# Kernel optimization log

Measured on AMD Instinct MI355X. Metric: run time of the kernel, lower is better.

## Reference

```python
import jax, jax.numpy as jnp
import numpy as np

HEADS = 12
HEAD_DIM = 64  # dim=768 // heads=12
NEG = -1e9


def setup_inputs() -> dict:
    key = jax.random.key(0)
    k1, k2, k3 = jax.random.split(key, 3)
    dim = HEADS * HEAD_DIM
    x = jax.random.normal(k1, (8, 1024, dim), dtype=jnp.float32)
    W_qkv = jax.random.normal(k2, (dim, 3 * dim), dtype=jnp.float32) * (dim ** -0.5)
    b_qkv = jnp.zeros((3 * dim,), dtype=jnp.float32)
    W_out = jax.random.normal(k3, (dim, dim), dtype=jnp.float32) * (dim ** -0.5)
    b_out = jnp.zeros((dim,), dtype=jnp.float32)
    return {"x": x, "W_qkv": W_qkv, "b_qkv": b_qkv, "W_out": W_out, "b_out": b_out}


def reference(x, W_qkv, b_qkv, W_out, b_out):
    B, T, C = x.shape
    qkv = x @ W_qkv + b_qkv                      # [B,T,3C]
    q, k, v = jnp.split(qkv, 3, axis=-1)
    # [B,T,C] -> [B,H,T,Dh]
    def split_heads(t):
        return t.reshape(B, T, HEADS, HEAD_DIM).transpose(0, 2, 1, 3)
    q, k, v = split_heads(q), split_heads(k), split_heads(v)
    att = jnp.einsum('bhqd,bhkd->bhqk', q, k) / jnp.sqrt(jnp.float32(HEAD_DIM))
    causal = jnp.tril(jnp.ones((T, T), dtype=bool))  # [T,T]
    att = jnp.where(causal[None, None], att, NEG)
    att = jax.nn.softmax(att, axis=-1)
    out = jnp.einsum('bhqk,bhkd->bhqd', att, v)  # [B,H,T,Dh]
    out = out.transpose(0, 2, 1, 3).reshape(B, T, C)
    return out @ W_out + b_out
```

## Files before the change

kernel.cpp:

```cpp
#include <hip/hip_runtime.h>
#include <hip/hip_bf16.h>

typedef unsigned short u16;
typedef unsigned int u32;
typedef __attribute__((ext_vector_type(8))) short short8;
typedef __attribute__((ext_vector_type(4))) float f32x4;
typedef __attribute__((ext_vector_type(16))) float f32x16;
typedef __attribute__((ext_vector_type(4))) unsigned int uint4v;

__device__ __forceinline__ u16 f2bf(float f) {
    union { float f; unsigned int u; } v; v.f = f;
    unsigned int u = v.u;
    return (u16)((u + 0x7FFFu + ((u >> 16) & 1u)) >> 16);
}
__device__ __forceinline__ u32 pk2(float a, float b) {
    return ((u32)f2bf(b) << 16) | (u32)f2bf(a);
}

__global__ void k_convert(const float* __restrict__ x, u16* __restrict__ o, int n4) {
    int i = blockIdx.x * blockDim.x + threadIdx.x;
    if (i < n4) {
        float4 v = ((const float4*)x)[i];
        ushort4 r;
        r.x = f2bf(v.x); r.y = f2bf(v.y); r.z = f2bf(v.z); r.w = f2bf(v.w);
        ((ushort4*)o)[i] = r;
    }
}

__global__ void k_transpose_bf(const float* __restrict__ W, u16* __restrict__ Wt, int K, int N) {
    __shared__ u16 t[32][33];
    int n0 = blockIdx.x * 32, k0 = blockIdx.y * 32;
    int tx = threadIdx.x, ty = threadIdx.y;
    #pragma unroll
    for (int i = 0; i < 4; i++) {
        t[ty + i * 8][tx] = f2bf(W[(long)(k0 + ty + i * 8) * N + n0 + tx]);
    }
    __syncthreads();
    #pragma unroll
    for (int i = 0; i < 4; i++) {
        Wt[(long)(n0 + ty + i * 8) * K + k0 + tx] = t[tx][ty + i * 8];
    }
}

__global__ void k_vt(const u16* __restrict__ qkv, u16* __restrict__ vt) {
    __shared__ u16 s[32][33];
    int t0 = blockIdx.x * 32, d0 = blockIdx.y * 32, bh = blockIdx.z;
    int b = bh / 12, h = bh - b * 12;
    int tx = threadIdx.x, ty = threadIdx.y;
    const u16* src = qkv + (size_t)(b * 1024 + t0) * 2304 + 1536 + h * 64 + d0;
    #pragma unroll
    for (int i = 0; i < 4; i++) {
        s[ty + i * 8][tx] = src[(size_t)(ty + i * 8) * 2304 + tx];
    }
    __syncthreads();
    u16* dst = vt + (size_t)bh * 65536 + (size_t)d0 * 1024 + t0;
    #pragma unroll
    for (int i = 0; i < 4; i++) {
        dst[(size_t)(ty + i * 8) * 1024 + tx] = s[tx][ty + i * 8];
    }
}

template<int EPI>
__global__ __launch_bounds__(256) void k_gemm_bt(
    const u16* __restrict__ A, const u16* __restrict__ Bt, const float* __restrict__ bias,
    float* __restrict__ Cf, u16* __restrict__ Cb,
    int M, int N, int K)
{
    __shared__ u16 lA[128][40];
    __shared__ u16 lB[128][40];
    int tid = threadIdx.x;
    int wid = tid >> 6, lane = tid & 63;
    int wm = wid >> 1, wn = wid & 1;
    int ln = lane & 15, gp = lane >> 4;
    int gm0 = blockIdx.x * 128, gn0 = blockIdx.y * 128;

    f32x4 zf = {0.f, 0.f, 0.f, 0.f};
    f32x4 acc[4][4];
    #pragma unroll
    for (int i = 0; i < 4; i++)
        #pragma unroll
        for (int j = 0; j < 4; j++) acc[i][j] = zf;

    int sr = tid >> 2;
    int sc = (tid & 3) * 8;

    for (int k0 = 0; k0 < K; k0 += 32) {
        #pragma unroll
        for (int j = 0; j < 2; j++) {
            int r = sr + j * 64;
            *(uint4v*)&lA[r][sc] = *(const uint4v*)&A[(long)(gm0 + r) * K + k0 + sc];
            *(uint4v*)&lB[r][sc] = *(const uint4v*)&Bt[(long)(gn0 + r) * K + k0 + sc];
        }
        __syncthreads();
        short8 af[4], bfr[4];
        #pragma unroll
        for (int i = 0; i < 4; i++) {
            af[i]  = *(const short8*)&lA[wm * 64 + i * 16 + ln][gp * 8];
            bfr[i] = *(const short8*)&lB[wn * 64 + i * 16 + ln][gp * 8];
        }
        #pragma unroll
        for (int i = 0; i < 4; i++)
            #pragma unroll
            for (int j = 0; j < 4; j++)
                acc[i][j] = __builtin_amdgcn_mfma_f32_16x16x32_bf16(af[i], bfr[j], acc[i][j], 0, 0, 0);
        __syncthreads();
    }

    #pragma unroll
    for (int i = 0; i < 4; i++) {
        #pragma unroll
        for (int j = 0; j < 4; j++) {
            #pragma unroll
            for (int r = 0; r < 4; r++) {
                int m = gm0 + wm * 64 + i * 16 + gp * 4 + r;
                int n = gn0 + wn * 64 + j * 16 + ln;
                float v = acc[i][j][r] + bias[n];
                if (EPI == 0) Cf[(long)m * N + n] = v;
                else          Cb[(long)m * N + n] = f2bf(v);
            }
        }
    }
}

__global__ __launch_bounds__(64) void k_attn(
    const u16* __restrict__ qkv, const u16* __restrict__ Vt,
    u16* __restrict__ O)
{
    int lane = threadIdx.x;
    int l31 = lane & 31, hi = lane >> 5;
    int bx = blockIdx.x;
    int qtq = bx / 96, bh = bx - qtq * 96;
    int qt = 31 - qtq, q0 = qt * 32;
    int b = bh / 12, h = bh - b * 12;
    const u16* Qb  = qkv + (size_t)(b * 1024) * 2304 + h * 64;
    const u16* Kbb = Qb + 768;
    const u16* Vb  = Vt + (size_t)bh * 65536;

    short8 qf[4];
    #pragma unroll
    for (int ch = 0; ch < 4; ch++)
        qf[ch] = *(const short8*)&Qb[(size_t)(q0 + l31) * 2304 + ch * 16 + hi * 8];

    f32x16 o0 = {}, o1 = {};
    float mrun = -INFINITY, lsum = 0.f;
    const float SC = 0.18033688011f;

    int nit = qt + 1;
    for (int it = 0; it < nit; it++) {
        int kt = it * 32;
        f32x16 sa = {}, sb = {};
        {
            short8 kf0 = *(const short8*)&Kbb[(size_t)(kt + l31) * 2304 + 0 * 16 + hi * 8];
            short8 kf1 = *(const short8*)&Kbb[(size_t)(kt + l31) * 2304 + 1 * 16 + hi * 8];
            short8 kf2 = *(const short8*)&Kbb[(size_t)(kt + l31) * 2304 + 2 * 16 + hi * 8];
            short8 kf3 = *(const short8*)&Kbb[(size_t)(kt + l31) * 2304 + 3 * 16 + hi * 8];
            sa = __builtin_amdgcn_mfma_f32_32x32x16_bf16(kf0, qf[0], sa, 0, 0, 0);
            sb = __builtin_amdgcn_mfma_f32_32x32x16_bf16(kf2, qf[2], sb, 0, 0, 0);
            sa = __builtin_amdgcn_mfma_f32_32x32x16_bf16(kf1, qf[1], sa, 0, 0, 0);
            sb = __builtin_amdgcn_mfma_f32_32x32x16_bf16(kf3, qf[3], sb, 0, 0, 0);
        }
        float ps[16];
        int qg = q0 + l31;
        #pragma unroll
        for (int r = 0; r < 16; r++) {
            int krow = kt + (r & 3) + 8 * (r >> 2) + 4 * hi;
            ps[r] = (krow <= qg) ? (sa[r] + sb[r]) * SC : -1e30f;
        }
        float t8[8];
        #pragma unroll
        for (int i = 0; i < 8; i++) t8[i] = fmaxf(ps[i], ps[i + 8]);
        float t4a = fmaxf(t8[0], t8[1]), t4b = fmaxf(t8[2], t8[3]);
        float t4c = fmaxf(t8[4], t8[5]), t4d = fmaxf(t8[6], t8[7]);
        float tm = fmaxf(fmaxf(t4a, t4b), fmaxf(t4c, t4d));
        tm = fmaxf(tm, __shfl_xor(tm, 32));
        float mn = fmaxf(mrun, tm);
        float scale = exp2f(mrun - mn);
        mrun = mn;
        float rs = 0.f;
        #pragma unroll
        for (int r = 0; r < 16; r++) { ps[r] = exp2f(ps[r] - mn); rs += ps[r]; }
        rs += __shfl_xor(rs, 32);
        lsum = lsum * scale + rs;
        #pragma unroll
        for (int r = 0; r < 16; r++) { o0[r] *= scale; o1[r] *= scale; }
        u32 c[8], sw[8];
        #pragma unroll
        for (int i = 0; i < 8; i++) c[i] = pk2(ps[2 * i], ps[2 * i + 1]);
        #pragma unroll
        for (int i = 0; i < 8; i++) sw[i] = (u32)__shfl_xor((int)c[i], 32);
        union { u32 u[4]; short8 s8; } pb0, pb1;
        pb0.u[0] = hi ? sw[2] : c[0];
        pb0.u[1] = hi ? sw[3] : c[1];
        pb0.u[2] = hi ? c[2]  : sw[0];
        pb0.u[3] = hi ? c[3]  : sw[1];
        pb1.u[0] = hi ? sw[6] : c[4];
        pb1.u[1] = hi ? sw[7] : c[5];
        pb1.u[2] = hi ? c[6]  : sw[4];
        pb1.u[3] = hi ? c[7]  : sw[5];
        #pragma unroll
        for (int kh = 0; kh < 2; kh++) {
            const short8* pbp = kh ? &pb1.s8 : &pb0.s8;
            short8 vf0 = *(const short8*)&Vb[(size_t)l31 * 1024 + kt + kh * 16 + hi * 8];
            short8 vf1 = *(const short8*)&Vb[(size_t)(32 + l31) * 1024 + kt + kh * 16 + hi * 8];
            o0 = __builtin_amdgcn_mfma_f32_32x32x16_bf16(vf0, *pbp, o0, 0, 0, 0);
            o1 = __builtin_amdgcn_mfma_f32_32x32x16_bf16(vf1, *pbp, o1, 0, 0, 0);
        }
    }

    float inv = 1.0f / lsum;
    int t = q0 + l31;
    size_t base = ((size_t)(b * 1024 + t)) * 768 + h * 64;
    #pragma unroll
    for (int rq = 0; rq < 4; rq++) {
        ushort4 u0, u1;
        u0.x = f2bf(o0[4 * rq + 0] * inv); u0.y = f2bf(o0[4 * rq + 1] * inv);
        u0.z = f2bf(o0[4 * rq + 2] * inv); u0.w = f2bf(o0[4 * rq + 3] * inv);
        u1.x = f2bf(o1[4 * rq + 0] * inv); u1.y = f2bf(o1[4 * rq + 1] * inv);
        u1.z = f2bf(o1[4 * rq + 2] * inv); u1.w = f2bf(o1[4 * rq + 3] * inv);
        *(ushort4*)&O[base + rq * 8 + hi * 4]      = u0;
        *(ushort4*)&O[base + 32 + rq * 8 + hi * 4] = u1;
    }
}

extern "C" void kernel_launch(void* const* d_in, const int* in_sizes, int n_in,
                              void* d_out, int out_size, void* d_ws, size_t ws_size,
                              hipStream_t stream)
{
    const float* x     = (const float*)d_in[0];
    const float* W_qkv = (const float*)d_in[1];
    const float* b_qkv = (const float*)d_in[2];
    const float* W_out = (const float*)d_in[3];
    const float* b_out = (const float*)d_in[4];
    float* out = (float*)d_out;

    char* w = (char*)d_ws;
    u16* xb   = (u16*)w; w += (size_t)8192 * 768 * 2;
    u16* wqt  = (u16*)w; w += (size_t)2304 * 768 * 2;
    u16* wot  = (u16*)w; w += (size_t)768 * 768 * 2;
    u16* qkv  = (u16*)w; w += (size_t)8192 * 2304 * 2;
    u16* vt   = (u16*)w; w += (size_t)96 * 64 * 1024 * 2;
    u16* ao   = (u16*)w; w += (size_t)8192 * 768 * 2;

    k_convert<<<dim3(6144), 256, 0, stream>>>(x, xb, 1572864);
    k_transpose_bf<<<dim3(72, 24), dim3(32, 8), 0, stream>>>(W_qkv, wqt, 768, 2304);
    k_transpose_bf<<<dim3(24, 24), dim3(32, 8), 0, stream>>>(W_out, wot, 768, 768);
    k_gemm_bt<2><<<dim3(64, 18), 256, 0, stream>>>(xb, wqt, b_qkv, nullptr, qkv, 8192, 2304, 768);
    k_vt<<<dim3(32, 2, 96), dim3(32, 8), 0, stream>>>(qkv, vt);
    k_attn<<<dim3(3072), 64, 0, stream>>>(qkv, vt, ao);
    k_gemm_bt<0><<<dim3(64, 6), 256, 0, stream>>>(ao, wot, b_out, out, nullptr, 8192, 768, 768);
}
```

Baseline: 151.7 us.

## Prefetch K/V tiles through swizzled LDS and apply lazy softmax rescaling

Loads the next K and V tiles into registers while computing the current one, then stages them in XOR-swizzled shared memory so MFMA operands come from LDS instead of strided global reads. Causal masking is now applied only on the diagonal tile. The online softmax skips rescaling of the accumulators unless the new max grows by more than a threshold, and folds the scale into an fma. This adds LDS traffic and register pressure from the prefetch buffers, and the larger unnormalized exponentials carry a small precision risk.

```diff
diff --git a/kernel.cpp b/kernel.cpp
--- a/kernel.cpp
+++ b/kernel.cpp
@@ -122,10 +122,12 @@
     }
 }
 
-__global__ __launch_bounds__(64) void k_attn(
+__global__ __launch_bounds__(64, 3) void k_attn(
     const u16* __restrict__ qkv, const u16* __restrict__ Vt,
     u16* __restrict__ O)
 {
+    __shared__ u16 sK[2048];
+    __shared__ u16 sV[2048];
     int lane = threadIdx.x;
     int l31 = lane & 31, hi = lane >> 5;
     int bx = blockIdx.x;
@@ -141,48 +143,93 @@
     for (int ch = 0; ch < 4; ch++)
         qf[ch] = *(const short8*)&Qb[(size_t)(q0 + l31) * 2304 + ch * 16 + hi * 8];
 
+    int rK = lane >> 3, cK = lane & 7;
+    int rV = lane >> 2, cV = lane & 3;
+
+    uint4v rk[4], rv[4];
+    auto gload = [&](int kt) {
+        #pragma unroll
+        for (int j = 0; j < 4; j++) {
+            int r = j * 8 + rK;
+            rk[j] = *(const uint4v*)&Kbb[(size_t)(kt + r) * 2304 + cK * 8];
+        }
+        #pragma unroll
+        for (int j = 0; j < 4; j++) {
+            int r = j * 16 + rV;
+            rv[j] = *(const uint4v*)&Vb[(size_t)r * 1024 + kt + cV * 8];
+        }
+    };
+    auto swrite = [&]() {
+        #pragma unroll
+        for (int j = 0; j < 4; j++) {
+            int r = j * 8 + rK;
+            *(uint4v*)&sK[r * 64 + ((cK ^ (r & 7)) * 8)] = rk[j];
+        }
+        #pragma unroll
+        for (int j = 0; j < 4; j++) {
+            int r = j * 16 + rV;
+            *(uint4v*)&sV[r * 32 + ((cV ^ (r & 3) ^ ((r >> 2) & 3)) * 8)] = rv[j];
+        }
+    };
+
     f32x16 o0 = {}, o1 = {};
     float mrun = -INFINITY, lsum = 0.f;
     const float SC = 0.18033688011f;
+    int swl = l31 & 7;
+    int swv = (l31 & 3) ^ ((l31 >> 2) & 3);
 
     int nit = qt + 1;
+    gload(0);
+    swrite();
     for (int it = 0; it < nit; it++) {
         int kt = it * 32;
+        if (it + 1 < nit) gload(kt + 32);
         f32x16 sa = {}, sb = {};
         {
-            short8 kf0 = *(const short8*)&Kbb[(size_t)(kt + l31) * 2304 + 0 * 16 + hi * 8];
-            short8 kf1 = *(const short8*)&Kbb[(size_t)(kt + l31) * 2304 + 1 * 16 + hi * 8];
-            short8 kf2 = *(const short8*)&Kbb[(size_t)(kt + l31) * 2304 + 2 * 16 + hi * 8];
-            short8 kf3 = *(const short8*)&Kbb[(size_t)(kt + l31) * 2304 + 3 * 16 + hi * 8];
+            short8 kf0 = *(const short8*)&sK[l31 * 64 + (((0 + hi) ^ swl) * 8)];
+            short8 kf1 = *(const short8*)&sK[l31 * 64 + (((2 + hi) ^ swl) * 8)];
+            short8 kf2 = *(const short8*)&sK[l31 * 64 + (((4 + hi) ^ swl) * 8)];
+            short8 kf3 = *(const short8*)&sK[l31 * 64 + (((6 + hi) ^ swl) * 8)];
             sa = __builtin_amdgcn_mfma_f32_32x32x16_bf16(kf0, qf[0], sa, 0, 0, 0);
             sb = __builtin_amdgcn_mfma_f32_32x32x16_bf16(kf2, qf[2], sb, 0, 0, 0);
             sa = __builtin_amdgcn_mfma_f32_32x32x16_bf16(kf1, qf[1], sa, 0, 0, 0);
             sb = __builtin_amdgcn_mfma_f32_32x32x16_bf16(kf3, qf[3], sb, 0, 0, 0);
         }
-        float ps[16];
-        int qg = q0 + l31;
-        #pragma unroll
-        for (int r = 0; r < 16; r++) {
-            int krow = kt + (r & 3) + 8 * (r >> 2) + 4 * hi;
-            ps[r] = (krow <= qg) ? (sa[r] + sb[r]) * SC : -1e30f;
+        float raw[16];
+        #pragma unroll
+        for (int r = 0; r < 16; r++) raw[r] = sa[r] + sb[r];
+        if (it == nit - 1) {
+            #pragma unroll
+            for (int r = 0; r < 16; r++) {
+                int crow = (r & 3) + 8 * (r >> 2) + 4 * hi;
+                raw[r] = (crow <= l31) ? raw[r] : -1e30f;
+            }
         }
         float t8[8];
         #pragma unroll
-        for (int i = 0; i < 8; i++) t8[i] = fmaxf(ps[i], ps[i + 8]);
+        for (int i = 0; i < 8; i++) t8[i] = fmaxf(raw[i], raw[i + 8]);
         float t4a = fmaxf(t8[0], t8[1]), t4b = fmaxf(t8[2], t8[3]);
         float t4c = fmaxf(t8[4], t8[5]), t4d = fmaxf(t8[6], t8[7]);
         float tm = fmaxf(fmaxf(t4a, t4b), fmaxf(t4c, t4d));
         tm = fmaxf(tm, __shfl_xor(tm, 32));
-        float mn = fmaxf(mrun, tm);
-        float scale = exp2f(mrun - mn);
-        mrun = mn;
+        float stm = tm * SC;
+        if (!__all(stm - mrun <= 8.0f)) {
+            float mn = fmaxf(mrun, stm);
+            float scale = exp2f(mrun - mn);
+            lsum *= scale;
+            #pragma unroll
+            for (int r = 0; r < 16; r++) { o0[r] *= scale; o1[r] *= scale; }
+            mrun = mn;
+        }
+        float ps[16];
         float rs = 0.f;
         #pragma unroll
-        for (int r = 0; r < 16; r++) { ps[r] = exp2f(ps[r] - mn); rs += ps[r]; }
+        for (int r = 0; r < 16; r++) {
+            ps[r] = exp2f(fmaf(raw[r], SC, -mrun));
+            rs += ps[r];
+        }
         rs += __shfl_xor(rs, 32);
-        lsum = lsum * scale + rs;
-        #pragma unroll
-        for (int r = 0; r < 16; r++) { o0[r] *= scale; o1[r] *= scale; }
+        lsum += rs;
         u32 c[8], sw[8];
         #pragma unroll
         for (int i = 0; i < 8; i++) c[i] = pk2(ps[2 * i], ps[2 * i + 1]);
@@ -200,11 +247,13 @@
         #pragma unroll
         for (int kh = 0; kh < 2; kh++) {
             const short8* pbp = kh ? &pb1.s8 : &pb0.s8;
-            short8 vf0 = *(const short8*)&Vb[(size_t)l31 * 1024 + kt + kh * 16 + hi * 8];
-            short8 vf1 = *(const short8*)&Vb[(size_t)(32 + l31) * 1024 + kt + kh * 16 + hi * 8];
+            int p = (((kh * 2 + hi) ^ swv) * 8);
+            short8 vf0 = *(const short8*)&sV[l31 * 32 + p];
+            short8 vf1 = *(const short8*)&sV[(32 + l31) * 32 + p];
             o0 = __builtin_amdgcn_mfma_f32_32x32x16_bf16(vf0, *pbp, o0, 0, 0, 0);
             o1 = __builtin_amdgcn_mfma_f32_32x32x16_bf16(vf1, *pbp, o1, 0, 0, 0);
         }
+        if (it + 1 < nit) swrite();
     }
 
     float inv = 1.0f / lsum;
```

Measured after the change: 135.7 us. -10.5%, faster.
